# Kernel optimization log

Measured on AMD Instinct MI355X. Metric: run time of the kernel, lower is better.

Reference implementation:

```python
import jax, jax.numpy as jnp
import numpy as np

N, K, D, CP, H, S, P = 8192, 32, 768, 128, 8, 64, 8
NPTS = 3 * P  # 2*query_points + value_points = 24 points per head
FEAT = H * CP + H * S + H * P * 3 + H * P  # 1792


def layer_norm(x, scale, offset, eps=1e-5):
    m = x.mean(-1, keepdims=True)
    v = ((x - m) ** 2).mean(-1, keepdims=True)
    return (x - m) * jax.lax.rsqrt(v + eps) * scale + offset


def frames_from_pos(pos):
    # Gram-Schmidt rigid frame from backbone N(0), CA(1), C(2) atoms (extract_aa_frames).
    n, ca, c = pos[:, 0], pos[:, 1], pos[:, 2]
    eps = 1e-8
    v1 = c - ca
    v2 = n - ca
    e1 = v1 * jax.lax.rsqrt((v1 ** 2).sum(-1, keepdims=True) + eps)
    u2 = v2 - (v2 * e1).sum(-1, keepdims=True) * e1
    e2 = u2 * jax.lax.rsqrt((u2 ** 2).sum(-1, keepdims=True) + eps)
    e3 = jnp.cross(e1, e2)
    R = jnp.stack([e1, e2, e3], axis=-1)  # [N,3,3], columns = frame axes
    return R, ca


def setup_inputs() -> dict:
    key = jax.random.key(0)
    ks = jax.random.split(key, 10)
    inp = {
        "local": jax.random.normal(ks[0], (N, D), jnp.float32),
        "pos": jax.random.normal(ks[1], (N, 14, 3), jnp.float32) * 3.0,
        "pair": jax.random.normal(ks[2], (N, K, CP), jnp.float32),
        "pair_mask": jnp.ones((N, K), bool),
        "neighbours": jax.random.randint(ks[3], (N, K), 0, N, dtype=jnp.int32),
        "resi": jnp.arange(N, dtype=jnp.int32),
        "chain": jnp.zeros((N,), jnp.int32),
        "batch": jnp.zeros((N,), jnp.int32),
        "mask": jnp.ones((N,), bool),
        # parameters
        "ln_local_s": jnp.ones((D,), jnp.float32),
        "ln_local_b": jnp.zeros((D,), jnp.float32),
        "W_qkv": jax.random.normal(ks[4], (D, H * 3 * S), jnp.float32) / np.sqrt(D),
        "ln_q_s": jnp.ones((S,), jnp.float32),
        "ln_q_b": jnp.zeros((S,), jnp.float32),
        "ln_k_s": jnp.ones((S,), jnp.float32),
        "ln_k_b": jnp.zeros((S,), jnp.float32),
        "W_pts": jax.random.normal(ks[5], (D, H * NPTS * 3), jnp.float32) / np.sqrt(D),
        "W_bias": jax.random.normal(ks[6], (CP, H), jnp.float32) / np.sqrt(CP),
        "gamma": jnp.full((H,), np.log(np.e - 1.0), jnp.float32),
        "W_out": jax.random.normal(ks[7], (FEAT, D), jnp.float32) / np.sqrt(FEAT),
        "b_out": jnp.zeros((D,), jnp.float32),
    }
    return inp


def reference(local, pos, pair, pair_mask, neighbours, resi, chain, batch, mask,
              ln_local_s, ln_local_b, W_qkv, ln_q_s, ln_q_b, ln_k_s, ln_k_b,
              W_pts, W_bias, gamma, W_out, b_out):
    R, t = frames_from_pos(pos)                       # [N,3,3], [N,3]
    x = layer_norm(local, ln_local_s, ln_local_b)     # normalize=True
    qkv = (x @ W_qkv).reshape(-1, H, 3 * S)
    q, k, v = jnp.split(qkv, 3, axis=-1)              # each [N,H,S]
    q = layer_norm(q, ln_q_s, ln_q_b)
    k = layer_norm(k, ln_k_s, ln_k_b)
    # points in global frame: p = R @ raw + t
    raw = (x @ W_pts).reshape(-1, H, NPTS, 3)
    pts = jnp.einsum('nij,nhpj->nhpi', R, raw) + t[:, None, None]
    q_g, k_g, v_g = jnp.split(pts, [P, 2 * P], axis=-2)  # [N,H,P,3] each
    bias = jnp.einsum('nkc,ch->nkh', pair, W_bias)
    w_C = jnp.sqrt(2.0 / (9.0 * P))
    w_L = jnp.sqrt(1.0 / 3.0)
    dfactor = jax.nn.softplus(gamma)[None, None] * w_C / 2.0  # [1,1,H]
    diff = q_g[:, None] - k_g[neighbours]              # [N,K,H,P,3]
    dist = dfactor * (diff ** 2).sum((-1, -2))         # [N,K,H]
    dot = jnp.sqrt(1.0 / S) * jnp.einsum('nhc,nkhc->nkh', q, k[neighbours])
    logits = w_L * (dot + bias - dist)
    pm = pair_mask & (neighbours != -1)
    logits = jnp.where(pm[..., None], logits, -1e9)
    attn = jax.nn.softmax(logits, axis=1)              # softmax over neighbours (axis=-2)
    attn = jnp.where(pm[..., None], attn, 0.0)
    out_pair = jnp.einsum('nkh,nkc->nhc', attn, pair)
    out_scalar = jnp.einsum('nkh,nkhc->nhc', attn, v[neighbours])
    op = jnp.einsum('nkh,nkhpc->nhpc', attn, v_g[neighbours])
    # back to local frame: R^T (p - t)
    op = jnp.einsum('nji,nhpj->nhpi', R, op - t[:, None, None])
    out_norm = jnp.sqrt((op ** 2).sum(-1) + 1e-8)      # [N,H,P]
    Nn = local.shape[0]
    feats = jnp.concatenate([
        out_pair.reshape(Nn, -1), out_scalar.reshape(Nn, -1),
        op.reshape(Nn, -1), out_norm.reshape(Nn, -1)], axis=-1)
    return feats @ W_out + b_out
```

## Files before the change

### kernel.cpp

```cpp
#include <hip/hip_runtime.h>
#include <hip/hip_bf16.h>


#define NN 8192
#define KNBR 32
#define DD 768
#define CPC 128
#define HH 8
#define FEATD 1792
#define QKVD 1536
#define PTSD 576
#define PAIR_ROW 4096

typedef __hip_bfloat16 bf16;
typedef __attribute__((ext_vector_type(8))) short s8;
typedef __attribute__((ext_vector_type(4))) float f4;
typedef __attribute__((ext_vector_type(4))) float fv4;

__device__ __forceinline__ float b2f(bf16 v) { return __bfloat162float(v); }
__device__ __forceinline__ bf16 f2b(float v) { return __float2bfloat16(v); }
__device__ __forceinline__ unsigned short f2u(float v) {
    bf16 h = __float2bfloat16(v);
    return *(unsigned short*)&h;
}
__device__ __forceinline__ void gl_lds16(const void* g, void* l) {
    __builtin_amdgcn_global_load_lds(
        (const __attribute__((address_space(1))) void*)g,
        (__attribute__((address_space(3))) void*)l, 16, 0, 0);
}

__device__ __forceinline__ void do_frames(int n, const float* __restrict__ pos,
                                          float* __restrict__ Rm,
                                          float* __restrict__ tv) {
    const float* p = pos + (size_t)n * 42;
    float nx[3], ca[3], cc[3];
#pragma unroll
    for (int j = 0; j < 3; ++j) { nx[j] = p[j]; ca[j] = p[3+j]; cc[j] = p[6+j]; }
    float v1[3], v2[3], e1[3], e2[3], e3[3];
#pragma unroll
    for (int j = 0; j < 3; ++j) { v1[j] = cc[j] - ca[j]; v2[j] = nx[j] - ca[j]; }
    float s1 = v1[0]*v1[0] + v1[1]*v1[1] + v1[2]*v1[2];
    float r1 = 1.0f / sqrtf(s1 + 1e-8f);
#pragma unroll
    for (int j = 0; j < 3; ++j) e1[j] = v1[j] * r1;
    float d = v2[0]*e1[0] + v2[1]*e1[1] + v2[2]*e1[2];
    float u2[3];
#pragma unroll
    for (int j = 0; j < 3; ++j) u2[j] = v2[j] - d * e1[j];
    float s2 = u2[0]*u2[0] + u2[1]*u2[1] + u2[2]*u2[2];
    float r2 = 1.0f / sqrtf(s2 + 1e-8f);
#pragma unroll
    for (int j = 0; j < 3; ++j) e2[j] = u2[j] * r2;
    e3[0] = e1[1]*e2[2] - e1[2]*e2[1];
    e3[1] = e1[2]*e2[0] - e1[0]*e2[2];
    e3[2] = e1[0]*e2[1] - e1[1]*e2[0];
#pragma unroll
    for (int i = 0; i < 3; ++i) {
        Rm[(size_t)n*9 + i*3 + 0] = e1[i];
        Rm[(size_t)n*9 + i*3 + 1] = e2[i];
        Rm[(size_t)n*9 + i*3 + 2] = e3[i];
        tv[(size_t)n*3 + i] = ca[i];
    }
}

__device__ __forceinline__ void do_transpose(const float* __restrict__ W,
                                             bf16* __restrict__ Wt,
                                             int K, int N, int group, int cn,
                                             int segsz, int rowoff,
                                             int bx, int by, int tid,
                                             char* shbuf) {
    bf16 (*tile)[33] = (bf16(*)[33])shbuf;
    int n0 = bx * 32, k0 = by * 32;
    int r = tid >> 5, c = tid & 31;
    for (int rr = r; rr < 32; rr += 8) {
        int n = n0 + c;
        tile[rr][c] = (n < N) ? f2b(W[(size_t)(k0 + rr) * N + n]) : f2b(0.0f);
    }
    __syncthreads();
    for (int rr = r; rr < 32; rr += 8) {
        int n = n0 + rr;
        int pn = n;
        if (cn != 0 && n < N) {
            int hh = n / group, rm = n % group;
            pn = (rm / cn) * segsz + hh * cn + (rm % cn);
        }
        Wt[(size_t)(rowoff + pn) * K + k0 + c] = tile[c][rr];
    }
}

__global__ __launch_bounds__(256) void prep_kernel(
        const float* __restrict__ local, const float* __restrict__ lns,
        const float* __restrict__ lnb, bf16* __restrict__ xln,
        const float* __restrict__ pos, float* __restrict__ Rm,
        float* __restrict__ tv,
        const float* __restrict__ W_qkv, const float* __restrict__ W_pts,
        bf16* __restrict__ wtm) {
    __shared__ __align__(16) char shbuf[2560];
    int b = blockIdx.x, tid = threadIdx.x;
    if (b < NN) {
        if (b < 32) do_frames(b * 256 + tid, pos, Rm, tv);
        float* red = (float*)shbuf;
        const float* row = local + (size_t)b * DD;
        float v[3];
#pragma unroll
        for (int e = 0; e < 3; ++e) v[e] = row[tid + 256*e];
        red[tid] = v[0] + v[1] + v[2];
        __syncthreads();
        for (int st = 128; st > 0; st >>= 1) {
            if (tid < st) red[tid] += red[tid + st];
            __syncthreads();
        }
        float mean = red[0] * (1.0f / DD);
        __syncthreads();
        float d0 = v[0]-mean, d1 = v[1]-mean, d2 = v[2]-mean;
        red[tid] = d0*d0 + d1*d1 + d2*d2;
        __syncthreads();
        for (int st = 128; st > 0; st >>= 1) {
            if (tid < st) red[tid] += red[tid + st];
            __syncthreads();
        }
        float rstd = rsqrtf(red[0] * (1.0f / DD) + 1e-5f);
        bf16* orow = xln + (size_t)b * DD;
#pragma unroll
        for (int e = 0; e < 3; ++e) {
            int c = tid + 256*e;
            orow[c] = f2b((v[e] - mean) * rstd * lns[c] + lnb[c]);
        }
    } else if (b < NN + 1152) {
        int t = b - NN;
        do_transpose(W_qkv, wtm, 768, 1536, 192, 64, 512, 0, t % 48, t / 48,
                     tid, shbuf);
    } else {
        int t = b - NN - 1152;
        do_transpose(W_pts, wtm, 768, PTSD, 72, 24, 192, 1536, t % 20, t / 20,
                     tid, shbuf);
    }
}

template<int SPLIT, int BIAS>
__global__ __launch_bounds__(256) void mfma_gemm(const bf16* __restrict__ A, int lda,
                                                 const bf16* __restrict__ Bt, int K,
                                                 void* __restrict__ C,
                                                 void* __restrict__ C2,
                                                 int ldc, int ncols,
                                                 const float* __restrict__ bias,
                                                 const float* __restrict__ lnqs,
                                                 const float* __restrict__ lnqb,
                                                 const float* __restrict__ lnks,
                                                 const float* __restrict__ lnkb,
                                                 const float* __restrict__ TW,
                                                 bf16* __restrict__ TWt,
                                                 int gemmBlocks, int gx) {
    __shared__ short As[128 * 64];
    __shared__ short Bs[128 * 64];
    int tid = threadIdx.x;
    int bid = blockIdx.x;

    if (TW != nullptr && bid >= gemmBlocks) {
        int t = bid - gemmBlocks;
        do_transpose(TW, TWt, FEATD, DD, 0, 0, 0, 0, t % 24, t / 24,
                     tid, (char*)As);
        return;
    }

    int w = tid >> 6, lane = tid & 63;
    int q = lane >> 4, lr = lane & 15;
    int cpx = gemmBlocks >> 3;
    int swz = (bid & 7) * cpx + (bid >> 3);
    int bx = swz % gx, by = swz / gx;
    int m0 = by * 128, n0 = bx * 128;
    int lrow = lane >> 3, lcol = (lane & 7) * 8;

    f4 acc[4][4] = {};

    for (int k0 = 0; k0 < K; k0 += 64) {
#pragma unroll
        for (int i = 0; i < 4; ++i) {
            int c = w * 4 + i;
            int r = c * 8 + lrow;
            gl_lds16(A  + (size_t)(m0 + r) * lda + k0 + lcol, As + c * 512);
            gl_lds16(Bt + (size_t)(n0 + r) * K   + k0 + lcol, Bs + c * 512);
        }
        __syncthreads();

#pragma unroll
        for (int kk = 0; kk < 2; ++kk) {
            const short* Ab = As + ((w & 1) * 64 + lr) * 64 + kk * 32 + q * 8;
            const short* Bb = Bs + ((w >> 1) * 64 + lr) * 64 + kk * 32 + q * 8;
            s8 af[4], bfr[4];
#pragma unroll
            for (int i = 0; i < 4; ++i) af[i] = *(const s8*)(Ab + i * 16 * 64);
#pragma unroll
            for (int j = 0; j < 4; ++j) bfr[j] = *(const s8*)(Bb + j * 16 * 64);
#pragma unroll
            for (int i = 0; i < 4; ++i)
#pragma unroll
                for (int j = 0; j < 4; ++j)
                    acc[i][j] = __builtin_amdgcn_mfma_f32_16x16x32_bf16(
                        af[i], bfr[j], acc[i][j], 0, 0, 0);
        }
        __syncthreads();
    }

    int mb = m0 + (w & 1) * 64, nb = n0 + (w >> 1) * 64;
    if (!SPLIT) {
#pragma unroll
        for (int i = 0; i < 4; ++i)
#pragma unroll
            for (int j = 0; j < 4; ++j) {
                int col = nb + j * 16 + lr;
                int row0 = mb + i * 16 + q * 4;
                if (col < ncols) {
#pragma unroll
                    for (int r = 0; r < 4; ++r) {
                        float v = acc[i][j][r];
                        if (BIAS) v += bias[col];
                        ((float*)C)[(size_t)(row0 + r) * ldc + col] = v;
                    }
                }
            }
    } else if (nb < 1024) {
        const float* sc = (nb < 512) ? lnqs : lnks;
        const float* of = (nb < 512) ? lnqb : lnkb;
        float scv[4], ofv[4];
#pragma unroll
        for (int j = 0; j < 4; ++j) { scv[j] = sc[j*16 + lr]; ofv[j] = of[j*16 + lr]; }
#pragma unroll
        for (int i = 0; i < 4; ++i) {
#pragma unroll
            for (int r = 0; r < 4; ++r) {
                float s = acc[i][0][r] + acc[i][1][r] + acc[i][2][r] + acc[i][3][r];
                s += __shfl_xor(s, 1, 64); s += __shfl_xor(s, 2, 64);
                s += __shfl_xor(s, 4, 64); s += __shfl_xor(s, 8, 64);
                float mean = s * (1.0f / 64.0f);
                float d0 = acc[i][0][r] - mean, d1 = acc[i][1][r] - mean;
                float d2 = acc[i][2][r] - mean, d3 = acc[i][3][r] - mean;
                float vs = d0*d0 + d1*d1 + d2*d2 + d3*d3;
                vs += __shfl_xor(vs, 1, 64); vs += __shfl_xor(vs, 2, 64);
                vs += __shfl_xor(vs, 4, 64); vs += __shfl_xor(vs, 8, 64);
                float rstd = rsqrtf(vs * (1.0f / 64.0f) + 1e-5f);
                unsigned short* Crow =
                    (unsigned short*)C + (size_t)(mb + i*16 + q*4 + r) * QKVD + nb;
                Crow[0*16 + lr] = f2u(d0 * rstd * scv[0] + ofv[0]);
                Crow[1*16 + lr] = f2u(d1 * rstd * scv[1] + ofv[1]);
                Crow[2*16 + lr] = f2u(d2 * rstd * scv[2] + ofv[2]);
                Crow[3*16 + lr] = f2u(d3 * rstd * scv[3] + ofv[3]);
            }
        }
    } else if (nb < QKVD) {
#pragma unroll
        for (int i = 0; i < 4; ++i)
#pragma unroll
            for (int j = 0; j < 4; ++j) {
                int col = nb + j * 16 + lr;
                int row0 = mb + i * 16 + q * 4;
#pragma unroll
                for (int r = 0; r < 4; ++r)
                    ((unsigned short*)C)[(size_t)(row0 + r) * QKVD + col] =
                        f2u(acc[i][j][r]);
            }
    } else {
#pragma unroll
        for (int i = 0; i < 4; ++i)
#pragma unroll
            for (int j = 0; j < 4; ++j) {
                int col = nb + j * 16 + lr;
                int row0 = mb + i * 16 + q * 4;
                if (col - QKVD < PTSD) {
                    int pc = col - QKVD;
#pragma unroll
                    for (int r = 0; r < 4; ++r)
                        ((float*)C2)[(size_t)(row0 + r) * PTSD + pc] = acc[i][j][r];
                }
            }
    }
}

__global__ __launch_bounds__(256) void rotate_pts_kernel(float* __restrict__ pts,
                                                         const float* __restrict__ Rm,
                                                         const float* __restrict__ tv) {
    int idx = blockIdx.x * blockDim.x + threadIdx.x;
    if (idx >= NN * 192) return;
    int n = idx / 192;
    int rem = idx % 192;
    float* base = pts + (size_t)n * PTSD + rem * 3;
    float r0 = base[0], r1 = base[1], r2 = base[2];
    const float* R = Rm + (size_t)n * 9;
    const float* t = tv + (size_t)n * 3;
    base[0] = R[0]*r0 + R[1]*r1 + R[2]*r2 + t[0];
    base[1] = R[3]*r0 + R[4]*r1 + R[5]*r2 + t[1];
    base[2] = R[6]*r0 + R[7]*r1 + R[8]*r2 + t[2];
}

__global__ __launch_bounds__(256) void attn_kernel(const bf16* __restrict__ qkv,
                                                   const float* __restrict__ pts,
                                                   const float* __restrict__ Rm,
                                                   const float* __restrict__ tv,
                                                   float* __restrict__ pair,
                                                   const int* __restrict__ nbr,
                                                   const float* __restrict__ Wb,
                                                   const float* __restrict__ gamma) {
    int n = blockIdx.x;
    int tid = threadIdx.x;
    int w = tid >> 6, lane = tid & 63;
    int h = lane >> 3, cg = lane & 7;

    __shared__ float pairS[32][132];
    __shared__ float logitS[32][8];
    __shared__ float attnS[32][8];
    __shared__ float gS[192];
    __shared__ int nbS[32];
    __shared__ float dfS[8];

    const fv4* pr4 = (const fv4*)(pair + (size_t)n * PAIR_ROW);
    fv4 pv[4];
#pragma unroll
    for (int i = 0; i < 4; ++i) pv[i] = __builtin_nontemporal_load(pr4 + tid + 256*i);

    const int* nrow = nbr + (size_t)n * KNBR + w * 8;
    int nb_[8];
#pragma unroll
    for (int kk = 0; kk < 8; ++kk) nb_[kk] = nrow[kk];

    uint4 kv[8];
#pragma unroll
    for (int kk = 0; kk < 8; ++kk)
        kv[kk] = *(const uint4*)(qkv + (size_t)nb_[kk] * QKVD + 512 + h * 64 + cg * 8);
    fv4 kg[8];
    if (cg < 6) {
#pragma unroll
        for (int kk = 0; kk < 8; ++kk)
            kg[kk] = *(const fv4*)(pts + (size_t)nb_[kk] * PTSD + 192 + h * 24 + cg * 4);
    } else {
#pragma unroll
        for (int kk = 0; kk < 8; ++kk) kg[kk] = (fv4)(0.0f);
    }

    float qreg[8];
    {
        uint4 qv = *(const uint4*)(qkv + (size_t)n * QKVD + h * 64 + cg * 8);
        const unsigned short* qs = (const unsigned short*)&qv;
#pragma unroll
        for (int j = 0; j < 8; ++j) qreg[j] = b2f(*(const bf16*)&qs[j]);
    }
    fv4 qg = (fv4)(0.0f);
    if (cg < 6) qg = *(const fv4*)(pts + (size_t)n * PTSD + h * 24 + cg * 4);
    float wb[16];
#pragma unroll
    for (int j = 0; j < 16; ++j) wb[j] = Wb[(cg + 8 * j) * 8 + h];

#pragma unroll
    for (int i = 0; i < 4; ++i) {
        int e = tid + 256 * i;
        *(fv4*)&pairS[e >> 5][(e & 31) * 4] = pv[i];
    }
    if (tid < 32) nbS[tid] = nbr[(size_t)n * KNBR + tid];
    if (tid < 8) dfS[tid] = log1pf(expf(gamma[tid])) * (1.0f / 12.0f);

    float pdot[8], pd2[8];
#pragma unroll
    for (int kk = 0; kk < 8; ++kk) {
        const unsigned short* ks = (const unsigned short*)&kv[kk];
        float dot = 0.0f;
#pragma unroll
        for (int j = 0; j < 8; ++j) dot += qreg[j] * b2f(*(const bf16*)&ks[j]);
        pdot[kk] = dot;
        float dx = qg.x - kg[kk].x, dy = qg.y - kg[kk].y;
        float dz = qg.z - kg[kk].z, dw = qg.w - kg[kk].w;
        pd2[kk] = dx*dx + dy*dy + dz*dz + dw*dw;
    }
    __syncthreads();

#pragma unroll
    for (int kk = 0; kk < 8; ++kk) {
        int k = w * 8 + kk;
        float bias = 0.0f;
#pragma unroll
        for (int j = 0; j < 16; ++j) bias += pairS[k][cg + 8 * j] * wb[j];
        float val = 0.125f * pdot[kk] + bias - dfS[h] * pd2[kk];
        val += __shfl_xor(val, 1, 64);
        val += __shfl_xor(val, 2, 64);
        val += __shfl_xor(val, 4, 64);
        if (cg == 0) logitS[k][h] = 0.5773502691896258f * val;
    }
    __syncthreads();

    if (tid < 64) {
        int hh = tid >> 3, j = tid & 7;
        float l[4];
        float m = -1e30f;
#pragma unroll
        for (int i = 0; i < 4; ++i) { l[i] = logitS[j + 8 * i][hh]; m = fmaxf(m, l[i]); }
        m = fmaxf(m, __shfl_xor(m, 1, 64));
        m = fmaxf(m, __shfl_xor(m, 2, 64));
        m = fmaxf(m, __shfl_xor(m, 4, 64));
        float s = 0.0f;
#pragma unroll
        for (int i = 0; i < 4; ++i) { l[i] = expf(l[i] - m); s += l[i]; }
        s += __shfl_xor(s, 1, 64);
        s += __shfl_xor(s, 2, 64);
        s += __shfl_xor(s, 4, 64);
        float inv = 1.0f / s;
#pragma unroll
        for (int i = 0; i < 4; ++i) attnS[j + 8 * i][hh] = l[i] * inv;
    }
    __syncthreads();

    bf16* fr = (bf16*)(pair + (size_t)n * PAIR_ROW);
    for (int e = tid; e < 1024; e += 256) {
        int hh = e >> 7, c = e & 127;
        float acc = 0.0f;
#pragma unroll
        for (int k = 0; k < KNBR; ++k) acc += attnS[k][hh] * pairS[k][c];
        fr[e] = f2b(acc);
    }
    if (tid < 64) {
        int hh = lane >> 3, c8 = (lane & 7) * 8;
        float a8[8] = {};
#pragma unroll
        for (int k = 0; k < KNBR; ++k) {
            float a = attnS[k][hh];
            uint4 vv = *(const uint4*)(qkv + (size_t)nbS[k] * QKVD + 1024 + hh * 64 + c8);
            const unsigned short* vs = (const unsigned short*)&vv;
#pragma unroll
            for (int j = 0; j < 8; ++j) a8[j] += a * b2f(*(const bf16*)&vs[j]);
        }
        unsigned short o[8];
#pragma unroll
        for (int j = 0; j < 8; ++j) o[j] = f2u(a8[j]);
        *(uint4*)(fr + 1024 + hh * 64 + c8) = *(const uint4*)o;
    } else {
        int t = tid - 64;
        int hh = t / 24;
        float acc = 0.0f;
#pragma unroll
        for (int k = 0; k < KNBR; ++k)
            acc += attnS[k][hh] * pts[(size_t)nbS[k] * PTSD + 384 + t];
        gS[t] = acc;
    }
    __syncthreads();
    if (tid < 64) {
        int hh = tid >> 3, p = tid & 7;
        const float* t = tv + (size_t)n * 3;
        const float* R = Rm + (size_t)n * 9;
        float gx = gS[hh * 24 + p * 3 + 0] - t[0];
        float gy = gS[hh * 24 + p * 3 + 1] - t[1];
        float gz = gS[hh * 24 + p * 3 + 2] - t[2];
        float o0 = R[0]*gx + R[3]*gy + R[6]*gz;
        float o1 = R[1]*gx + R[4]*gy + R[7]*gz;
        float o2 = R[2]*gx + R[5]*gy + R[8]*gz;
        fr[1536 + hh*24 + p*3 + 0] = f2b(o0);
        fr[1536 + hh*24 + p*3 + 1] = f2b(o1);
        fr[1536 + hh*24 + p*3 + 2] = f2b(o2);
        fr[1728 + hh*8 + p] = f2b(sqrtf(o0*o0 + o1*o1 + o2*o2 + 1e-8f));
    }
}

extern "C" void kernel_launch(void* const* d_in, const int* in_sizes, int n_in,
                              void* d_out, int out_size, void* d_ws, size_t ws_size,
                              hipStream_t stream) {
    const float* local      = (const float*)d_in[0];
    const float* pos        = (const float*)d_in[1];
    float*       pair       = (float*)d_in[2];
    const int*   neighbours = (const int*)d_in[4];
    const float* ln_s   = (const float*)d_in[9];
    const float* ln_b   = (const float*)d_in[10];
    const float* W_qkv  = (const float*)d_in[11];
    const float* ln_q_s = (const float*)d_in[12];
    const float* ln_q_b = (const float*)d_in[13];
    const float* ln_k_s = (const float*)d_in[14];
    const float* ln_k_b = (const float*)d_in[15];
    const float* W_pts  = (const float*)d_in[16];
    const float* W_bias = (const float*)d_in[17];
    const float* gamma  = (const float*)d_in[18];
    const float* W_out  = (const float*)d_in[19];
    const float* b_out  = (const float*)d_in[20];
    float* out = (float*)d_out;

    float* Rm   = (float*)d_ws;
    float* tv   = Rm   + (size_t)NN * 9;
    float* pts  = tv   + (size_t)NN * 3;
    bf16*  qkv  = (bf16*)(pts + (size_t)NN * PTSD);
    bf16*  xln  = (bf16*)d_out;
    bf16*  wtm  = xln + (size_t)NN * DD;
    bf16*  wt3  = (bf16*)local;

    prep_kernel<<<NN + 1152 + 480, 256, 0, stream>>>(
        local, ln_s, ln_b, xln, pos, Rm, tv, W_qkv, W_pts, wtm);

    mfma_gemm<1, 0><<<1088 + 1344, 256, 0, stream>>>(
        xln, DD, wtm, DD, qkv, pts, 0, 2176, nullptr,
        ln_q_s, ln_q_b, ln_k_s, ln_k_b, W_out, wt3, 1088, 17);

    rotate_pts_kernel<<<(NN * 192) / 256, 256, 0, stream>>>(pts, Rm, tv);

    attn_kernel<<<NN, 256, 0, stream>>>(qkv, pts, Rm, tv, pair, neighbours,
                                        W_bias, gamma);

    mfma_gemm<0, 1><<<384, 256, 0, stream>>>(
        (const bf16*)pair, PAIR_ROW * 2, wt3, FEATD, out, nullptr, DD, DD, b_out,
        nullptr, nullptr, nullptr, nullptr, nullptr, nullptr, 384, 6);
}
```

Measured before the change: 472.5 us.

## Double-buffer GEMM LDS tiles and use wave-shuffle single-pass layernorm

Result: faster. 457.4 us (-3.2%).

```diff
diff --git a/kernel.cpp b/kernel.cpp
--- a/kernel.cpp
+++ b/kernel.cpp
@@ -99,27 +99,26 @@
     int b = blockIdx.x, tid = threadIdx.x;
     if (b < NN) {
         if (b < 32) do_frames(b * 256 + tid, pos, Rm, tv);
-        float* red = (float*)shbuf;
+        int w = tid >> 6;
         const float* row = local + (size_t)b * DD;
         float v[3];
 #pragma unroll
         for (int e = 0; e < 3; ++e) v[e] = row[tid + 256*e];
-        red[tid] = v[0] + v[1] + v[2];
+        float s  = v[0] + v[1] + v[2];
+        float ss = v[0]*v[0] + v[1]*v[1] + v[2]*v[2];
+#pragma unroll
+        for (int m = 32; m > 0; m >>= 1) {
+            s  += __shfl_xor(s,  m, 64);
+            ss += __shfl_xor(ss, m, 64);
+        }
+        float* red = (float*)shbuf;
+        if ((tid & 63) == 0) { red[w] = s; red[4 + w] = ss; }
         __syncthreads();
-        for (int st = 128; st > 0; st >>= 1) {
-            if (tid < st) red[tid] += red[tid + st];
-            __syncthreads();
-        }
-        float mean = red[0] * (1.0f / DD);
-        __syncthreads();
-        float d0 = v[0]-mean, d1 = v[1]-mean, d2 = v[2]-mean;
-        red[tid] = d0*d0 + d1*d1 + d2*d2;
-        __syncthreads();
-        for (int st = 128; st > 0; st >>= 1) {
-            if (tid < st) red[tid] += red[tid + st];
-            __syncthreads();
-        }
-        float rstd = rsqrtf(red[0] * (1.0f / DD) + 1e-5f);
+        float S  = red[0] + red[1] + red[2] + red[3];
+        float SS = red[4] + red[5] + red[6] + red[7];
+        float mean = S * (1.0f / DD);
+        float var  = SS * (1.0f / DD) - mean * mean;
+        float rstd = rsqrtf(var + 1e-5f);
         bf16* orow = xln + (size_t)b * DD;
 #pragma unroll
         for (int e = 0; e < 3; ++e) {
@@ -151,8 +150,8 @@
                                                  const float* __restrict__ TW,
                                                  bf16* __restrict__ TWt,
                                                  int gemmBlocks, int gx) {
-    __shared__ short As[128 * 64];
-    __shared__ short Bs[128 * 64];
+    __shared__ short As[2][128 * 32];
+    __shared__ short Bs[2][128 * 32];
     int tid = threadIdx.x;
     int bid = blockIdx.x;
 
@@ -169,36 +168,41 @@
     int swz = (bid & 7) * cpx + (bid >> 3);
     int bx = swz % gx, by = swz / gx;
     int m0 = by * 128, n0 = bx * 128;
-    int lrow = lane >> 3, lcol = (lane & 7) * 8;
+    int lrow = lane >> 2, lcol = (lane & 3) * 8;
 
     f4 acc[4][4] = {};
 
-    for (int k0 = 0; k0 < K; k0 += 64) {
-#pragma unroll
-        for (int i = 0; i < 4; ++i) {
-            int c = w * 4 + i;
-            int r = c * 8 + lrow;
-            gl_lds16(A  + (size_t)(m0 + r) * lda + k0 + lcol, As + c * 512);
-            gl_lds16(Bt + (size_t)(n0 + r) * K   + k0 + lcol, Bs + c * 512);
+    auto stage = [&](int k0, int bsel) {
+#pragma unroll
+        for (int i = 0; i < 2; ++i) {
+            int c = w * 2 + i;
+            int r = c * 16 + lrow;
+            gl_lds16(A  + (size_t)(m0 + r) * lda + k0 + lcol, As[bsel] + c * 512);
+            gl_lds16(Bt + (size_t)(n0 + r) * K   + k0 + lcol, Bs[bsel] + c * 512);
         }
-        __syncthreads();
-
-#pragma unroll
-        for (int kk = 0; kk < 2; ++kk) {
-            const short* Ab = As + ((w & 1) * 64 + lr) * 64 + kk * 32 + q * 8;
-            const short* Bb = Bs + ((w >> 1) * 64 + lr) * 64 + kk * 32 + q * 8;
-            s8 af[4], bfr[4];
-#pragma unroll
-            for (int i = 0; i < 4; ++i) af[i] = *(const s8*)(Ab + i * 16 * 64);
-#pragma unroll
-            for (int j = 0; j < 4; ++j) bfr[j] = *(const s8*)(Bb + j * 16 * 64);
-#pragma unroll
-            for (int i = 0; i < 4; ++i)
-#pragma unroll
-                for (int j = 0; j < 4; ++j)
-                    acc[i][j] = __builtin_amdgcn_mfma_f32_16x16x32_bf16(
-                        af[i], bfr[j], acc[i][j], 0, 0, 0);
-        }
+    };
+
+    stage(0, 0);
+    __syncthreads();
+
+    int nt = K >> 5;
+    for (int t = 0; t < nt; ++t) {
+        if (t + 1 < nt) stage((t + 1) << 5, (t + 1) & 1);
+
+        const short* Ab = As[t & 1] + ((w & 1) * 64 + lr) * 32 + q * 8;
+        const short* Bb = Bs[t & 1] + ((w >> 1) * 64 + lr) * 32 + q * 8;
+        s8 af[4], bfr[4];
+#pragma unroll
+        for (int i = 0; i < 4; ++i) af[i] = *(const s8*)(Ab + i * 16 * 32);
+#pragma unroll
+        for (int j = 0; j < 4; ++j) bfr[j] = *(const s8*)(Bb + j * 16 * 32);
+#pragma unroll
+        for (int i = 0; i < 4; ++i)
+#pragma unroll
+            for (int j = 0; j < 4; ++j)
+                acc[i][j] = __builtin_amdgcn_mfma_f32_16x16x32_bf16(
+                    af[i], bfr[j], acc[i][j], 0, 0, 0);
+
         __syncthreads();
     }
 
```
